# Performance work log

Measured on AMD Instinct MI355X. Metric: run time of the kernel, lower is better.

## Reference

```python
import jax, jax.numpy as jnp
import numpy as np

D_MODEL = 1024
N_HEADS = 16
HEAD_DIM = D_MODEL // N_HEADS
EPS = 1e-6


def setup_inputs() -> dict:
    key = jax.random.key(0)
    ks = jax.random.split(key, 5)
    b, s = 2, 2048
    x = jax.random.normal(ks[0], (b, s, D_MODEL), dtype=jnp.float32)
    scale = 1.0 / np.sqrt(D_MODEL)
    Wq = jax.random.normal(ks[1], (D_MODEL, D_MODEL), dtype=jnp.float32) * scale
    Wk = jax.random.normal(ks[2], (D_MODEL, D_MODEL), dtype=jnp.float32) * scale
    Wv = jax.random.normal(ks[3], (D_MODEL, D_MODEL), dtype=jnp.float32) * scale
    Wo = jax.random.normal(ks[4], (D_MODEL, D_MODEL), dtype=jnp.float32) * scale
    return {"x": x, "Wq": Wq, "Wk": Wk, "Wv": Wv, "Wo": Wo}


def _feature_map(t):
    return jax.nn.relu(t) + EPS


def reference(x, Wq, Wk, Wv, Wo):
    b, s, _ = x.shape
    # nn.Linear applies x @ W.T
    q = (x @ Wq.T).reshape(b, s, N_HEADS, HEAD_DIM)
    k = (x @ Wk.T).reshape(b, s, N_HEADS, HEAD_DIM)
    v = (x @ Wv.T).reshape(b, s, N_HEADS, HEAD_DIM)
    q = _feature_map(q).transpose(0, 2, 1, 3)  # bhsd
    k = _feature_map(k).transpose(0, 2, 1, 3)  # bhsd
    v = v.transpose(0, 2, 1, 3)                # bhsm
    # cumulative KV outer products: (b,h,s,d,m)
    kv = jnp.einsum('bhsd,bhsm->bhsdm', k, v)
    kv_cum = jnp.cumsum(kv, axis=2)
    out = jnp.einsum('bhsd,bhsdm->bhsm', q, kv_cum)
    k_cum = jnp.cumsum(k, axis=2)
    z = 1.0 / (jnp.einsum('bhsd,bhsd->bhs', q, k_cum) + EPS)
    out = out * z[..., None]
    out = out.transpose(0, 2, 1, 3).reshape(b, s, D_MODEL)
    return out @ Wo.T
```

## Files before the change

kernel.cpp:

```cpp
#include <hip/hip_runtime.h>

#define EPSF 1e-6f

typedef short bf16x8_t __attribute__((ext_vector_type(8)));
typedef float f32x4_t __attribute__((ext_vector_type(4)));

__device__ __forceinline__ ushort f2bf(float f) {
  union { float f; uint32_t u; } c; c.f = f;
  return (ushort)((c.u + 0x7FFFu + ((c.u >> 16) & 1u)) >> 16);
}
__device__ __forceinline__ float bf2f(ushort u) {
  union { uint32_t u; float f; } c; c.u = ((uint32_t)u) << 16;
  return c.f;
}

#define SWB(row, kbyte) (((row) << 7) + ((kbyte) ^ (((row) & 7) << 4)))

__global__ __launch_bounds__(256) void cvt5_kernel(
    const float4* __restrict__ x, const float4* __restrict__ wq,
    const float4* __restrict__ wk, const float4* __restrict__ wv,
    const float4* __restrict__ wo,
    ushort4* __restrict__ xb, ushort4* __restrict__ wqb,
    ushort4* __restrict__ wkb, ushort4* __restrict__ wvb,
    ushort4* __restrict__ wob)
{
  const int i = blockIdx.x * 256 + threadIdx.x;
  const float4* src; ushort4* dst; int off;
  if (i < (1 << 20)) { src = x; dst = xb; off = i; }
  else {
    const int j = i - (1 << 20);
    const int r = j >> 18;
    off = j & ((1 << 18) - 1);
    src = (r == 0) ? wq : (r == 1) ? wk : (r == 2) ? wv : wo;
    dst = (r == 0) ? wqb : (r == 1) ? wkb : (r == 2) ? wvb : wob;
  }
  const float4 v = src[off];
  ushort4 o;
  o.x = f2bf(v.x); o.y = f2bf(v.y); o.z = f2bf(v.z); o.w = f2bf(v.w);
  dst[off] = o;
}

template<int RELU, int OUT_BF16>
__device__ __forceinline__ void gemm_bt_mfma(
    const ushort* __restrict__ A, const ushort* __restrict__ B,
    void* __restrict__ C, const int K, const int N,
    const int row0, const int col0)
{
  __shared__ __align__(16) ushort As[2][128 * 32];
  __shared__ __align__(16) ushort Bs[2][128 * 32];
  const int tid = threadIdx.x;
  const int lane = tid & 63;
  const int wv = tid >> 6;
  const int wr = (wv >> 1) * 64;
  const int wc = (wv & 1) * 64;

  f32x4_t acc[4][4];
#pragma unroll
  for (int m = 0; m < 4; ++m)
#pragma unroll
    for (int n = 0; n < 4; ++n) acc[m][n] = (f32x4_t){0.f, 0.f, 0.f, 0.f};

  const int fr = lane & 15;
  const int kh = (lane >> 4) * 8;

  const int chunk0 = wv * 64 + lane;
  const int chunk1 = chunk0 + 256;
  const int rowA0 = chunk0 >> 2, kpA0 = (chunk0 & 3) << 3;
  const int rowA1 = chunk1 >> 2, kpA1 = (chunk1 & 3) << 3;
  const int ldoff0 = (wv * 64) * 8;
  const int ldoff1 = (wv * 64 + 256) * 8;

#define STAGE(buf, k0)                                                        \
  do {                                                                        \
    __builtin_amdgcn_global_load_lds(                                         \
        (const __attribute__((address_space(1))) void*)(A +                   \
            (size_t)(row0 + rowA0) * K + (k0) + kpA0),                        \
        (__attribute__((address_space(3))) void*)(&As[buf][ldoff0]), 16, 0, 0);\
    __builtin_amdgcn_global_load_lds(                                         \
        (const __attribute__((address_space(1))) void*)(B +                   \
            (size_t)(col0 + rowA0) * K + (k0) + kpA0),                        \
        (__attribute__((address_space(3))) void*)(&Bs[buf][ldoff0]), 16, 0, 0);\
    __builtin_amdgcn_global_load_lds(                                         \
        (const __attribute__((address_space(1))) void*)(A +                   \
            (size_t)(row0 + rowA1) * K + (k0) + kpA1),                        \
        (__attribute__((address_space(3))) void*)(&As[buf][ldoff1]), 16, 0, 0);\
    __builtin_amdgcn_global_load_lds(                                         \
        (const __attribute__((address_space(1))) void*)(B +                   \
            (size_t)(col0 + rowA1) * K + (k0) + kpA1),                        \
        (__attribute__((address_space(3))) void*)(&Bs[buf][ldoff1]), 16, 0, 0);\
  } while (0)

#define COMPUTE(buf)                                                          \
  do {                                                                        \
    bf16x8_t af[4], bfr[4];                                                   \
    _Pragma("unroll")                                                         \
    for (int m = 0; m < 4; ++m)                                               \
      af[m] = *(const bf16x8_t*)&As[buf][(wr + m * 16 + fr) * 32 + kh];       \
    _Pragma("unroll")                                                         \
    for (int n = 0; n < 4; ++n)                                               \
      bfr[n] = *(const bf16x8_t*)&Bs[buf][(wc + n * 16 + fr) * 32 + kh];      \
    __builtin_amdgcn_s_setprio(1);                                            \
    _Pragma("unroll")                                                         \
    for (int m = 0; m < 4; ++m)                                               \
      _Pragma("unroll")                                                       \
      for (int n = 0; n < 4; ++n)                                             \
        acc[m][n] = __builtin_amdgcn_mfma_f32_16x16x32_bf16(                  \
            af[m], bfr[n], acc[m][n], 0, 0, 0);                               \
    __builtin_amdgcn_s_setprio(0);                                            \
  } while (0)

  const int NT = K >> 5;
  STAGE(0, 0);
  __syncthreads();
  for (int t = 0; t < NT - 2; t += 2) {
    STAGE(1, (t + 1) << 5);
    COMPUTE(0);
    __syncthreads();
    STAGE(0, (t + 2) << 5);
    COMPUTE(1);
    __syncthreads();
  }
  STAGE(1, (NT - 1) << 5);
  COMPUTE(0);
  __syncthreads();
  COMPUTE(1);

#undef STAGE
#undef COMPUTE

  const int rq = (lane >> 4) * 4;
#pragma unroll
  for (int m = 0; m < 4; ++m) {
#pragma unroll
    for (int r = 0; r < 4; ++r) {
      const size_t grow = (size_t)(row0 + wr + m * 16 + rq + r);
#pragma unroll
      for (int n = 0; n < 4; ++n) {
        float val = acc[m][n][r];
        if (RELU) val = fmaxf(val, 0.f) + EPSF;
        const size_t gcol = (size_t)(col0 + wc + n * 16 + fr);
        if (OUT_BF16) ((ushort*)C)[grow * N + gcol] = f2bf(val);
        else          ((float*)C)[grow * N + gcol] = val;
      }
    }
  }
}

__global__ __launch_bounds__(256) void qkv_gemm_kernel(
    const ushort* __restrict__ xb,
    const ushort* __restrict__ wqb, const ushort* __restrict__ wkb,
    const ushort* __restrict__ wvb,
    ushort* __restrict__ q, ushort* __restrict__ k, ushort* __restrict__ v)
{
  const int which = blockIdx.y >> 3;
  const int bcol = blockIdx.y & 7;
  const ushort* B = (which == 0) ? wqb : (which == 1) ? wkb : wvb;
  ushort* C = (which == 0) ? q : (which == 1) ? k : v;
  if (which < 2)
    gemm_bt_mfma<1, 1>(xb, B, C, 1024, 1024, blockIdx.x * 128, bcol * 128);
  else
    gemm_bt_mfma<0, 1>(xb, B, C, 1024, 1024, blockIdx.x * 128, bcol * 128);
}

__global__ __launch_bounds__(256) void out_gemm_kernel(
    const ushort* __restrict__ at, const ushort* __restrict__ wob,
    float* __restrict__ out)
{
  gemm_bt_mfma<0, 0>(at, wob, out, 1024, 1024, blockIdx.x * 128, blockIdx.y * 128);
}


__global__ __launch_bounds__(256) void chunk_sums_kernel(
    const ushort* __restrict__ kbuf, const ushort* __restrict__ vbuf,
    float* __restrict__ kvsum, float* __restrict__ ksum)
{
  __shared__ __align__(16) ushort Kt[64 * 64];
  __shared__ __align__(16) ushort Vt[64 * 64];
  const int chunk = blockIdx.x;
  const int seq = blockIdx.y;
  const int b = seq >> 4, h = seq & 15;
  const int tid = threadIdx.x;
  const size_t base = ((size_t)b * 2048 + chunk * 64) * 1024 + h * 64;

#pragma unroll
  for (int r = 0; r < 2; ++r) {
    const int idx = tid + (r << 8);
    const int j = idx >> 3;
    const int e0 = (idx & 7) << 3;
    const bf16x8_t kv8 = *(const bf16x8_t*)(kbuf + base + (size_t)j * 1024 + e0);
    const bf16x8_t vv8 = *(const bf16x8_t*)(vbuf + base + (size_t)j * 1024 + e0);
#pragma unroll
    for (int t = 0; t < 8; ++t) {
      *(ushort*)((char*)Kt + SWB(e0 + t, j * 2)) = (ushort)kv8[t];
      *(ushort*)((char*)Vt + SWB(e0 + t, j * 2)) = (ushort)vv8[t];
    }
  }
  __syncthreads();

  if (tid < 64) {
    float s = 0.f;
#pragma unroll
    for (int g = 0; g < 8; ++g) {
      const bf16x8_t kr = *(const bf16x8_t*)((char*)Kt + SWB(tid, g * 16));
#pragma unroll
      for (int t = 0; t < 8; ++t) s += bf2f((ushort)kr[t]);
    }
    ksum[((size_t)seq * 32 + chunk) * 64 + tid] = s;
  }

  const int lane = tid & 63;
  const int wv = tid >> 6;
  const int wm = (wv >> 1) * 32;
  const int wd = (wv & 1) * 32;
  const int fr = lane & 15;
  const int khb = (lane >> 4) * 16;

  f32x4_t acc[2][2];
#pragma unroll
  for (int m = 0; m < 2; ++m)
#pragma unroll
    for (int n = 0; n < 2; ++n) acc[m][n] = (f32x4_t){0.f, 0.f, 0.f, 0.f};

#pragma unroll
  for (int kk = 0; kk < 2; ++kk) {
    bf16x8_t av[2], bk[2];
#pragma unroll
    for (int m = 0; m < 2; ++m)
      av[m] = *(const bf16x8_t*)((char*)Vt + SWB(wm + m * 16 + fr, kk * 64 + khb));
#pragma unroll
    for (int n = 0; n < 2; ++n)
      bk[n] = *(const bf16x8_t*)((char*)Kt + SWB(wd + n * 16 + fr, kk * 64 + khb));
#pragma unroll
    for (int m = 0; m < 2; ++m)
#pragma unroll
      for (int n = 0; n < 2; ++n)
        acc[m][n] = __builtin_amdgcn_mfma_f32_16x16x32_bf16(
            av[m], bk[n], acc[m][n], 0, 0, 0);
  }

  const size_t kvbase = ((size_t)seq * 32 + chunk) << 12;
  const int rq = (lane >> 4) * 4;
#pragma unroll
  for (int m = 0; m < 2; ++m)
#pragma unroll
    for (int r = 0; r < 4; ++r) {
      const int mrow = wm + m * 16 + rq + r;
#pragma unroll
      for (int n = 0; n < 2; ++n) {
        const int dcol = wd + n * 16 + fr;
        kvsum[kvbase + (size_t)mrow * 64 + dcol] = acc[m][n][r];
      }
    }
}

__global__ __launch_bounds__(256) void scan_kernel(
    float* __restrict__ kvsum, float* __restrict__ ksum)
{
  const int slice = blockIdx.x & 15;
  const int seq = blockIdx.x >> 4;
  const int e = slice * 256 + threadIdx.x;
  const size_t base = ((size_t)seq << 17) + e;
  float vals[32];
#pragma unroll
  for (int c = 0; c < 32; ++c) vals[c] = kvsum[base + ((size_t)c << 12)];
  float run = 0.f;
#pragma unroll
  for (int c = 0; c < 32; ++c) {
    const float t = vals[c];
    kvsum[base + ((size_t)c << 12)] = run;
    run += t;
  }
  if (slice == 0 && threadIdx.x < 64) {
    const size_t kb = (size_t)seq * 2048 + threadIdx.x;
    float kv2[32];
#pragma unroll
    for (int c = 0; c < 32; ++c) kv2[c] = ksum[kb + (size_t)c * 64];
    float run2 = 0.f;
#pragma unroll
    for (int c = 0; c < 32; ++c) {
      const float t = kv2[c];
      ksum[kb + (size_t)c * 64] = run2;
      run2 += t;
    }
  }
}

__global__ __launch_bounds__(256) void attn_chunk_kernel(
    const ushort* __restrict__ qbuf, const ushort* __restrict__ kbuf,
    const ushort* __restrict__ vbuf, const float* __restrict__ kvsum,
    const float* __restrict__ ksum, ushort* __restrict__ attn)
{
  __shared__ __align__(16) ushort Qs[64 * 64];
  __shared__ __align__(16) ushort Ks[64 * 64];
  __shared__ __align__(16) ushort Vt[64 * 64];
  __shared__ __align__(16) ushort Pl[64 * 64];
  __shared__ float ksp[64];
  __shared__ float zinv[64];
  const int chunk = blockIdx.x;
  const int seq = blockIdx.y;
  const int b = seq >> 4, h = seq & 15;
  const int tid = threadIdx.x;
  const size_t base = ((size_t)b * 2048 + chunk * 64) * 1024 + h * 64;

#pragma unroll
  for (int r = 0; r < 2; ++r) {
    const int idx = tid + (r << 8);
    const int row = idx >> 3;
    const int e0 = (idx & 7) << 3;
    const int kb = e0 << 1;
    *(bf16x8_t*)((char*)Qs + SWB(row, kb)) =
        *(const bf16x8_t*)(qbuf + base + (size_t)row * 1024 + e0);
    *(bf16x8_t*)((char*)Ks + SWB(row, kb)) =
        *(const bf16x8_t*)(kbuf + base + (size_t)row * 1024 + e0);
    const bf16x8_t vv8 = *(const bf16x8_t*)(vbuf + base + (size_t)row * 1024 + e0);
#pragma unroll
    for (int t = 0; t < 8; ++t)
      *(ushort*)((char*)Vt + SWB(e0 + t, row * 2)) = (ushort)vv8[t];
  }
  if (tid < 64) ksp[tid] = ksum[((size_t)seq * 32 + chunk) * 64 + tid];
  __syncthreads();

  const int lane = tid & 63;
  const int wv = tid >> 6;
  const int wr = (wv >> 1) * 32;
  const int wc = (wv & 1) * 32;
  const int fr = lane & 15;
  const int khb = (lane >> 4) * 16;
  const int rq = (lane >> 4) * 4;

  f32x4_t sf[2][2];
#pragma unroll
  for (int m = 0; m < 2; ++m)
#pragma unroll
    for (int n = 0; n < 2; ++n) sf[m][n] = (f32x4_t){0.f, 0.f, 0.f, 0.f};
#pragma unroll
  for (int kk = 0; kk < 2; ++kk) {
    bf16x8_t aq[2], bk[2];
#pragma unroll
    for (int m = 0; m < 2; ++m)
      aq[m] = *(const bf16x8_t*)((char*)Qs + SWB(wr + m * 16 + fr, kk * 64 + khb));
#pragma unroll
    for (int n = 0; n < 2; ++n)
      bk[n] = *(const bf16x8_t*)((char*)Ks + SWB(wc + n * 16 + fr, kk * 64 + khb));
#pragma unroll
    for (int m = 0; m < 2; ++m)
#pragma unroll
      for (int n = 0; n < 2; ++n)
        sf[m][n] = __builtin_amdgcn_mfma_f32_16x16x32_bf16(
            aq[m], bk[n], sf[m][n], 0, 0, 0);
  }
  __syncthreads();

#pragma unroll
  for (int m = 0; m < 2; ++m)
#pragma unroll
    for (int r = 0; r < 4; ++r) {
      const int i = wr + m * 16 + rq + r;
#pragma unroll
      for (int n = 0; n < 2; ++n) {
        const int j = wc + n * 16 + fr;
        const float pv = (j <= i) ? sf[m][n][r] : 0.f;
        *(ushort*)((char*)Pl + SWB(i, j * 2)) = f2bf(pv);
      }
    }
  const size_t kvbase = ((size_t)seq * 32 + chunk) << 12;
#pragma unroll
  for (int r = 0; r < 2; ++r) {
    const int idx = tid + (r << 8);
    const int mrow = idx >> 3;
    const int d0 = (idx & 7) << 3;
    const float4 lo = *(const float4*)(kvsum + kvbase + (size_t)mrow * 64 + d0);
    const float4 hi = *(const float4*)(kvsum + kvbase + (size_t)mrow * 64 + d0 + 4);
    bf16x8_t kv8;
    kv8[0] = (short)f2bf(lo.x); kv8[1] = (short)f2bf(lo.y);
    kv8[2] = (short)f2bf(lo.z); kv8[3] = (short)f2bf(lo.w);
    kv8[4] = (short)f2bf(hi.x); kv8[5] = (short)f2bf(hi.y);
    kv8[6] = (short)f2bf(hi.z); kv8[7] = (short)f2bf(hi.w);
    *(bf16x8_t*)((char*)Ks + SWB(mrow, d0 << 1)) = kv8;
  }
  __syncthreads();

  if (tid < 64) {
    const int i = tid;
    float dsum = 0.f, ssum = 0.f;
#pragma unroll
    for (int g = 0; g < 8; ++g) {
      const bf16x8_t qr = *(const bf16x8_t*)((char*)Qs + SWB(i, g * 16));
      const bf16x8_t pr = *(const bf16x8_t*)((char*)Pl + SWB(i, g * 16));
#pragma unroll
      for (int t = 0; t < 8; ++t) {
        dsum = fmaf(bf2f((ushort)qr[t]), ksp[g * 8 + t], dsum);
        ssum += bf2f((ushort)pr[t]);
      }
    }
    zinv[i] = 1.f / (dsum + ssum + EPSF);
  }

  f32x4_t of[2][2];
#pragma unroll
  for (int m = 0; m < 2; ++m)
#pragma unroll
    for (int n = 0; n < 2; ++n) of[m][n] = (f32x4_t){0.f, 0.f, 0.f, 0.f};
#pragma unroll
  for (int kk = 0; kk < 2; ++kk) {
    bf16x8_t ap[2], bv[2];
#pragma unroll
    for (int m = 0; m < 2; ++m)
      ap[m] = *(const bf16x8_t*)((char*)Pl + SWB(wr + m * 16 + fr, kk * 64 + khb));
#pragma unroll
    for (int n = 0; n < 2; ++n)
      bv[n] = *(const bf16x8_t*)((char*)Vt + SWB(wc + n * 16 + fr, kk * 64 + khb));
#pragma unroll
    for (int m = 0; m < 2; ++m)
#pragma unroll
      for (int n = 0; n < 2; ++n)
        of[m][n] = __builtin_amdgcn_mfma_f32_16x16x32_bf16(
            ap[m], bv[n], of[m][n], 0, 0, 0);
  }
#pragma unroll
  for (int kk = 0; kk < 2; ++kk) {
    bf16x8_t aq[2], bkv[2];
#pragma unroll
    for (int m = 0; m < 2; ++m)
      aq[m] = *(const bf16x8_t*)((char*)Qs + SWB(wr + m * 16 + fr, kk * 64 + khb));
#pragma unroll
    for (int n = 0; n < 2; ++n)
      bkv[n] = *(const bf16x8_t*)((char*)Ks + SWB(wc + n * 16 + fr, kk * 64 + khb));
#pragma unroll
    for (int m = 0; m < 2; ++m)
#pragma unroll
      for (int n = 0; n < 2; ++n)
        of[m][n] = __builtin_amdgcn_mfma_f32_16x16x32_bf16(
            aq[m], bkv[n], of[m][n], 0, 0, 0);
  }
  __syncthreads();

#pragma unroll
  for (int m = 0; m < 2; ++m)
#pragma unroll
    for (int r = 0; r < 4; ++r) {
      const int i = wr + m * 16 + rq + r;
      const float z = zinv[i];
#pragma unroll
      for (int n = 0; n < 2; ++n) {
        const int mcol = wc + n * 16 + fr;
        attn[base + (size_t)i * 1024 + mcol] = f2bf(of[m][n][r] * z);
      }
    }
}

extern "C" void kernel_launch(void* const* d_in, const int* in_sizes, int n_in,
                              void* d_out, int out_size, void* d_ws, size_t ws_size,
                              hipStream_t stream)
{
  (void)in_sizes; (void)n_in; (void)out_size; (void)ws_size;
  const float* x  = (const float*)d_in[0];
  const float* Wq = (const float*)d_in[1];
  const float* Wk = (const float*)d_in[2];
  const float* Wv = (const float*)d_in[3];
  const float* Wo = (const float*)d_in[4];
  float* out = (float*)d_out;

  const size_t NM = (size_t)4096 * 1024;
  ushort* xb  = (ushort*)d_ws;
  ushort* wqb = xb + NM;
  ushort* wkb = wqb + (1 << 20);
  ushort* wvb = wkb + (1 << 20);
  ushort* wob = wvb + (1 << 20);
  ushort* qb  = wob + (1 << 20);
  ushort* kb  = qb + NM;
  ushort* vb  = kb + NM;
  ushort* at  = vb + NM;
  float*  ksm = (float*)(at + NM);
  float*  kvs = (float*)d_out;

  cvt5_kernel<<<8192, 256, 0, stream>>>(
      (const float4*)x, (const float4*)Wq, (const float4*)Wk,
      (const float4*)Wv, (const float4*)Wo,
      (ushort4*)xb, (ushort4*)wqb, (ushort4*)wkb, (ushort4*)wvb, (ushort4*)wob);
  qkv_gemm_kernel<<<dim3(32, 24), 256, 0, stream>>>(xb, wqb, wkb, wvb, qb, kb, vb);
  chunk_sums_kernel<<<dim3(32, 32), 256, 0, stream>>>(kb, vb, kvs, ksm);
  scan_kernel<<<512, 256, 0, stream>>>(kvs, ksm);
  attn_chunk_kernel<<<dim3(32, 32), 256, 0, stream>>>(qb, kb, vb, kvs, ksm, at);
  out_gemm_kernel<<<dim3(32, 8), 256, 0, stream>>>(at, wob, out);
}
```

Before: 180.7 us.

## Use 64-wide swizzled K tiles in GEMMs and split-K the output projection

The shared GEMM helper now stages K tiles of 64 instead of 32, using an XOR-swizzled LDS layout to avoid bank conflicts, which halves the number of barriers per K loop. The output projection is split along K into two halves across a new grid dimension, and partial results are combined with float atomicAdd into an output that is zeroed beforehand with a memset. This doubles the block count for the under-occupied 256-block output GEMM. The cost is atomic traffic, an extra memset, a different workspace location for the KV sums (moved off d_out), and doubled LDS per block, which may reduce occupancy.

```diff
diff --git a/kernel.cpp b/kernel.cpp
--- a/kernel.cpp
+++ b/kernel.cpp
@@ -40,14 +40,15 @@
   dst[off] = o;
 }
 
-template<int RELU, int OUT_BF16>
+template<int RELU, int OUT_BF16, int ATOMIC>
 __device__ __forceinline__ void gemm_bt_mfma(
     const ushort* __restrict__ A, const ushort* __restrict__ B,
-    void* __restrict__ C, const int K, const int N,
-    const int row0, const int col0)
-{
-  __shared__ __align__(16) ushort As[2][128 * 32];
-  __shared__ __align__(16) ushort Bs[2][128 * 32];
+    void* __restrict__ C, const int K,
+    const int kbeg, const int kend,
+    const int N, const int row0, const int col0)
+{
+  __shared__ __align__(16) ushort As[2][128 * 64];
+  __shared__ __align__(16) ushort Bs[2][128 * 64];
   const int tid = threadIdx.x;
   const int lane = tid & 63;
   const int wv = tid >> 6;
@@ -61,66 +62,72 @@
     for (int n = 0; n < 4; ++n) acc[m][n] = (f32x4_t){0.f, 0.f, 0.f, 0.f};
 
   const int fr = lane & 15;
-  const int kh = (lane >> 4) * 8;
-
-  const int chunk0 = wv * 64 + lane;
-  const int chunk1 = chunk0 + 256;
-  const int rowA0 = chunk0 >> 2, kpA0 = (chunk0 & 3) << 3;
-  const int rowA1 = chunk1 >> 2, kpA1 = (chunk1 & 3) << 3;
-  const int ldoff0 = (wv * 64) * 8;
-  const int ldoff1 = (wv * 64 + 256) * 8;
-
-#define STAGE(buf, k0)                                                        \
+
+  int rowc[4], scol[4], dsto[4];
+#pragma unroll
+  for (int is = 0; is < 4; ++is) {
+    const int c0 = is * 256 + tid;
+    rowc[is] = c0 >> 3;
+    scol[is] = (((c0 & 7) ^ ((c0 >> 3) & 7)) << 3);
+    dsto[is] = ((c0 >> 6) << 6) * 8;
+  }
+
+#define STAGE(buf, k0v)                                                       \
   do {                                                                        \
-    __builtin_amdgcn_global_load_lds(                                         \
-        (const __attribute__((address_space(1))) void*)(A +                   \
-            (size_t)(row0 + rowA0) * K + (k0) + kpA0),                        \
-        (__attribute__((address_space(3))) void*)(&As[buf][ldoff0]), 16, 0, 0);\
-    __builtin_amdgcn_global_load_lds(                                         \
-        (const __attribute__((address_space(1))) void*)(B +                   \
-            (size_t)(col0 + rowA0) * K + (k0) + kpA0),                        \
-        (__attribute__((address_space(3))) void*)(&Bs[buf][ldoff0]), 16, 0, 0);\
-    __builtin_amdgcn_global_load_lds(                                         \
-        (const __attribute__((address_space(1))) void*)(A +                   \
-            (size_t)(row0 + rowA1) * K + (k0) + kpA1),                        \
-        (__attribute__((address_space(3))) void*)(&As[buf][ldoff1]), 16, 0, 0);\
-    __builtin_amdgcn_global_load_lds(                                         \
-        (const __attribute__((address_space(1))) void*)(B +                   \
-            (size_t)(col0 + rowA1) * K + (k0) + kpA1),                        \
-        (__attribute__((address_space(3))) void*)(&Bs[buf][ldoff1]), 16, 0, 0);\
+    _Pragma("unroll")                                                         \
+    for (int is = 0; is < 4; ++is) {                                          \
+      __builtin_amdgcn_global_load_lds(                                       \
+          (const __attribute__((address_space(1))) void*)(A +                 \
+              (size_t)(row0 + rowc[is]) * K + (k0v) + scol[is]),              \
+          (__attribute__((address_space(3))) void*)(&As[buf][dsto[is]]),      \
+          16, 0, 0);                                                          \
+      __builtin_amdgcn_global_load_lds(                                       \
+          (const __attribute__((address_space(1))) void*)(B +                 \
+              (size_t)(col0 + rowc[is]) * K + (k0v) + scol[is]),              \
+          (__attribute__((address_space(3))) void*)(&Bs[buf][dsto[is]]),      \
+          16, 0, 0);                                                          \
+    }                                                                         \
   } while (0)
 
 #define COMPUTE(buf)                                                          \
   do {                                                                        \
-    bf16x8_t af[4], bfr[4];                                                   \
     _Pragma("unroll")                                                         \
-    for (int m = 0; m < 4; ++m)                                               \
-      af[m] = *(const bf16x8_t*)&As[buf][(wr + m * 16 + fr) * 32 + kh];       \
-    _Pragma("unroll")                                                         \
-    for (int n = 0; n < 4; ++n)                                               \
-      bfr[n] = *(const bf16x8_t*)&Bs[buf][(wc + n * 16 + fr) * 32 + kh];      \
-    __builtin_amdgcn_s_setprio(1);                                            \
-    _Pragma("unroll")                                                         \
-    for (int m = 0; m < 4; ++m)                                               \
+    for (int kk = 0; kk < 2; ++kk) {                                          \
+      bf16x8_t af[4], bfr[4];                                                 \
+      const int kb = kk * 64 + (lane & 48);                                   \
       _Pragma("unroll")                                                       \
-      for (int n = 0; n < 4; ++n)                                             \
-        acc[m][n] = __builtin_amdgcn_mfma_f32_16x16x32_bf16(                  \
-            af[m], bfr[n], acc[m][n], 0, 0, 0);                               \
-    __builtin_amdgcn_s_setprio(0);                                            \
+      for (int m = 0; m < 4; ++m) {                                           \
+        const int r_ = wr + m * 16 + fr;                                      \
+        af[m] = *(const bf16x8_t*)((const char*)As[buf] + SWB(r_, kb));       \
+      }                                                                       \
+      _Pragma("unroll")                                                       \
+      for (int n = 0; n < 4; ++n) {                                           \
+        const int r_ = wc + n * 16 + fr;                                      \
+        bfr[n] = *(const bf16x8_t*)((const char*)Bs[buf] + SWB(r_, kb));      \
+      }                                                                       \
+      __builtin_amdgcn_s_setprio(1);                                          \
+      _Pragma("unroll")                                                       \
+      for (int m = 0; m < 4; ++m)                                             \
+        _Pragma("unroll")                                                     \
+        for (int n = 0; n < 4; ++n)                                           \
+          acc[m][n] = __builtin_amdgcn_mfma_f32_16x16x32_bf16(                \
+              af[m], bfr[n], acc[m][n], 0, 0, 0);                             \
+      __builtin_amdgcn_s_setprio(0);                                          \
+    }                                                                         \
   } while (0)
 
-  const int NT = K >> 5;
-  STAGE(0, 0);
+  const int NT = (kend - kbeg) >> 6;
+  STAGE(0, kbeg);
   __syncthreads();
   for (int t = 0; t < NT - 2; t += 2) {
-    STAGE(1, (t + 1) << 5);
+    STAGE(1, kbeg + ((t + 1) << 6));
     COMPUTE(0);
     __syncthreads();
-    STAGE(0, (t + 2) << 5);
+    STAGE(0, kbeg + ((t + 2) << 6));
     COMPUTE(1);
     __syncthreads();
   }
-  STAGE(1, (NT - 1) << 5);
+  STAGE(1, kbeg + ((NT - 1) << 6));
   COMPUTE(0);
   __syncthreads();
   COMPUTE(1);
@@ -139,8 +146,9 @@
         float val = acc[m][n][r];
         if (RELU) val = fmaxf(val, 0.f) + EPSF;
         const size_t gcol = (size_t)(col0 + wc + n * 16 + fr);
-        if (OUT_BF16) ((ushort*)C)[grow * N + gcol] = f2bf(val);
-        else          ((float*)C)[grow * N + gcol] = val;
+        if (ATOMIC)        atomicAdd(&((float*)C)[grow * N + gcol], val);
+        else if (OUT_BF16) ((ushort*)C)[grow * N + gcol] = f2bf(val);
+        else               ((float*)C)[grow * N + gcol] = val;
       }
     }
   }
@@ -157,16 +165,20 @@
   const ushort* B = (which == 0) ? wqb : (which == 1) ? wkb : wvb;
   ushort* C = (which == 0) ? q : (which == 1) ? k : v;
   if (which < 2)
-    gemm_bt_mfma<1, 1>(xb, B, C, 1024, 1024, blockIdx.x * 128, bcol * 128);
+    gemm_bt_mfma<1, 1, 0>(xb, B, C, 1024, 0, 1024, 1024,
+                          blockIdx.x * 128, bcol * 128);
   else
-    gemm_bt_mfma<0, 1>(xb, B, C, 1024, 1024, blockIdx.x * 128, bcol * 128);
+    gemm_bt_mfma<0, 1, 0>(xb, B, C, 1024, 0, 1024, 1024,
+                          blockIdx.x * 128, bcol * 128);
 }
 
 __global__ __launch_bounds__(256) void out_gemm_kernel(
     const ushort* __restrict__ at, const ushort* __restrict__ wob,
     float* __restrict__ out)
 {
-  gemm_bt_mfma<0, 0>(at, wob, out, 1024, 1024, blockIdx.x * 128, blockIdx.y * 128);
+  const int kb0 = blockIdx.z * 512;
+  gemm_bt_mfma<0, 0, 1>(at, wob, out, 1024, kb0, kb0 + 512, 1024,
+                        blockIdx.x * 128, blockIdx.y * 128);
 }
 
 
@@ -453,7 +465,7 @@
                               void* d_out, int out_size, void* d_ws, size_t ws_size,
                               hipStream_t stream)
 {
-  (void)in_sizes; (void)n_in; (void)out_size; (void)ws_size;
+  (void)in_sizes; (void)n_in; (void)ws_size;
   const float* x  = (const float*)d_in[0];
   const float* Wq = (const float*)d_in[1];
   const float* Wk = (const float*)d_in[2];
@@ -472,7 +484,9 @@
   ushort* vb  = kb + NM;
   ushort* at  = vb + NM;
   float*  ksm = (float*)(at + NM);
-  float*  kvs = (float*)d_out;
+  float*  kvs = ksm + 65536;
+
+  hipMemsetAsync(d_out, 0, (size_t)out_size * sizeof(float), stream);
 
   cvt5_kernel<<<8192, 256, 0, stream>>>(
       (const float4*)x, (const float4*)Wq, (const float4*)Wk,
@@ -482,5 +496,5 @@
   chunk_sums_kernel<<<dim3(32, 32), 256, 0, stream>>>(kb, vb, kvs, ksm);
   scan_kernel<<<512, 256, 0, stream>>>(kvs, ksm);
   attn_chunk_kernel<<<dim3(32, 32), 256, 0, stream>>>(qb, kb, vb, kvs, ksm, at);
-  out_gemm_kernel<<<dim3(32, 8), 256, 0, stream>>>(at, wob, out);
-}
+  out_gemm_kernel<<<dim3(32, 8, 2), 256, 0, stream>>>(at, wob, out);
+}
```

After: 199.5 us. 1.1x slower.

## Store scanned KV prefix as bf16 and narrow out-GEMM tile to 128x64

Applied to the files above, without the earlier changes.

The scan kernel now writes the exclusive KV prefix sums directly as bf16 into a separate workspace buffer. The attention kernel therefore loads half the bytes and skips its per-element conversion. The output projection uses a 128x64 tile with twice as many blocks, giving more parallelism on a GPU with many CUs. The change also removes the setprio hints around the MFMA loop and turns the ReLU flag into a runtime bool, which merges the two QKV template instantiations but adds a branch in the epilogue.

```diff
diff --git a/kernel.cpp b/kernel.cpp
--- a/kernel.cpp
+++ b/kernel.cpp
@@ -40,73 +40,71 @@
   dst[off] = o;
 }
 
-template<int RELU, int OUT_BF16>
+template<int BN, int OUT_BF16>
 __device__ __forceinline__ void gemm_bt_mfma(
     const ushort* __restrict__ A, const ushort* __restrict__ B,
-    void* __restrict__ C, const int K, const int N,
-    const int row0, const int col0)
-{
-  __shared__ __align__(16) ushort As[2][128 * 32];
-  __shared__ __align__(16) ushort Bs[2][128 * 32];
+    void* __restrict__ C, const int K,
+    const int N, const int row0, const int col0, const bool relu)
+{
+  constexpr int NFR = BN / 32;
+  __shared__ __align__(16) uint As[2][2048];
+  __shared__ __align__(16) uint Bs[2][BN * 16];
   const int tid = threadIdx.x;
   const int lane = tid & 63;
   const int wv = tid >> 6;
   const int wr = (wv >> 1) * 64;
-  const int wc = (wv & 1) * 64;
-
-  f32x4_t acc[4][4];
+  const int wc = (wv & 1) * (BN / 2);
+
+  f32x4_t acc[4][NFR];
 #pragma unroll
   for (int m = 0; m < 4; ++m)
 #pragma unroll
-    for (int n = 0; n < 4; ++n) acc[m][n] = (f32x4_t){0.f, 0.f, 0.f, 0.f};
+    for (int n = 0; n < NFR; ++n) acc[m][n] = (f32x4_t){0.f, 0.f, 0.f, 0.f};
 
   const int fr = lane & 15;
   const int kh = (lane >> 4) * 8;
 
-  const int chunk0 = wv * 64 + lane;
-  const int chunk1 = chunk0 + 256;
-  const int rowA0 = chunk0 >> 2, kpA0 = (chunk0 & 3) << 3;
-  const int rowA1 = chunk1 >> 2, kpA1 = (chunk1 & 3) << 3;
-  const int ldoff0 = (wv * 64) * 8;
-  const int ldoff1 = (wv * 64 + 256) * 8;
-
-#define STAGE(buf, k0)                                                        \
+#define STAGE(buf, k0v)                                                       \
   do {                                                                        \
-    __builtin_amdgcn_global_load_lds(                                         \
-        (const __attribute__((address_space(1))) void*)(A +                   \
-            (size_t)(row0 + rowA0) * K + (k0) + kpA0),                        \
-        (__attribute__((address_space(3))) void*)(&As[buf][ldoff0]), 16, 0, 0);\
-    __builtin_amdgcn_global_load_lds(                                         \
-        (const __attribute__((address_space(1))) void*)(B +                   \
-            (size_t)(col0 + rowA0) * K + (k0) + kpA0),                        \
-        (__attribute__((address_space(3))) void*)(&Bs[buf][ldoff0]), 16, 0, 0);\
-    __builtin_amdgcn_global_load_lds(                                         \
-        (const __attribute__((address_space(1))) void*)(A +                   \
-            (size_t)(row0 + rowA1) * K + (k0) + kpA1),                        \
-        (__attribute__((address_space(3))) void*)(&As[buf][ldoff1]), 16, 0, 0);\
-    __builtin_amdgcn_global_load_lds(                                         \
-        (const __attribute__((address_space(1))) void*)(B +                   \
-            (size_t)(col0 + rowA1) * K + (k0) + kpA1),                        \
-        (__attribute__((address_space(3))) void*)(&Bs[buf][ldoff1]), 16, 0, 0);\
+    _Pragma("unroll")                                                         \
+    for (int is = 0; is < 2; ++is) {                                          \
+      const int c = tid + (is << 8);                                          \
+      const int row = c >> 2, kq = (c & 3) << 3;                              \
+      __builtin_amdgcn_global_load_lds(                                       \
+          (const __attribute__((address_space(1))) void*)(A +                 \
+              (size_t)(row0 + row) * K + (k0v) + kq),                         \
+          (__attribute__((address_space(3))) void*)(&As[buf][(c & ~63) * 4]), \
+          16, 0, 0);                                                          \
+    }                                                                         \
+    _Pragma("unroll")                                                         \
+    for (int is = 0; is < BN / 64; ++is) {                                    \
+      const int c = tid + (is << 8);                                          \
+      const int row = c >> 2, kq = (c & 3) << 3;                              \
+      __builtin_amdgcn_global_load_lds(                                       \
+          (const __attribute__((address_space(1))) void*)(B +                 \
+              (size_t)(col0 + row) * K + (k0v) + kq),                         \
+          (__attribute__((address_space(3))) void*)(&Bs[buf][(c & ~63) * 4]), \
+          16, 0, 0);                                                          \
+    }                                                                         \
   } while (0)
 
 #define COMPUTE(buf)                                                          \
   do {                                                                        \
-    bf16x8_t af[4], bfr[4];                                                   \
+    bf16x8_t af[4], bfr[NFR];                                                 \
     _Pragma("unroll")                                                         \
     for (int m = 0; m < 4; ++m)                                               \
-      af[m] = *(const bf16x8_t*)&As[buf][(wr + m * 16 + fr) * 32 + kh];       \
+      af[m] = *(const bf16x8_t*)((const ushort*)As[buf] +                     \
+                                 (size_t)(wr + m * 16 + fr) * 32 + kh);       \
     _Pragma("unroll")                                                         \
-    for (int n = 0; n < 4; ++n)                                               \
-      bfr[n] = *(const bf16x8_t*)&Bs[buf][(wc + n * 16 + fr) * 32 + kh];      \
-    __builtin_amdgcn_s_setprio(1);                                            \
+    for (int n = 0; n < NFR; ++n)                                             \
+      bfr[n] = *(const bf16x8_t*)((const ushort*)Bs[buf] +                    \
+                                  (size_t)(wc + n * 16 + fr) * 32 + kh);      \
     _Pragma("unroll")                                                         \
     for (int m = 0; m < 4; ++m)                                               \
       _Pragma("unroll")                                                       \
-      for (int n = 0; n < 4; ++n)                                             \
+      for (int n = 0; n < NFR; ++n)                                           \
         acc[m][n] = __builtin_amdgcn_mfma_f32_16x16x32_bf16(                  \
             af[m], bfr[n], acc[m][n], 0, 0, 0);                               \
-    __builtin_amdgcn_s_setprio(0);                                            \
   } while (0)
 
   const int NT = K >> 5;
@@ -135,9 +133,9 @@
     for (int r = 0; r < 4; ++r) {
       const size_t grow = (size_t)(row0 + wr + m * 16 + rq + r);
 #pragma unroll
-      for (int n = 0; n < 4; ++n) {
+      for (int n = 0; n < NFR; ++n) {
         float val = acc[m][n][r];
-        if (RELU) val = fmaxf(val, 0.f) + EPSF;
+        if (relu) val = fmaxf(val, 0.f) + EPSF;
         const size_t gcol = (size_t)(col0 + wc + n * 16 + fr);
         if (OUT_BF16) ((ushort*)C)[grow * N + gcol] = f2bf(val);
         else          ((float*)C)[grow * N + gcol] = val;
@@ -156,17 +154,16 @@
   const int bcol = blockIdx.y & 7;
   const ushort* B = (which == 0) ? wqb : (which == 1) ? wkb : wvb;
   ushort* C = (which == 0) ? q : (which == 1) ? k : v;
-  if (which < 2)
-    gemm_bt_mfma<1, 1>(xb, B, C, 1024, 1024, blockIdx.x * 128, bcol * 128);
-  else
-    gemm_bt_mfma<0, 1>(xb, B, C, 1024, 1024, blockIdx.x * 128, bcol * 128);
+  gemm_bt_mfma<128, 1>(xb, B, C, 1024, 1024,
+                       blockIdx.x * 128, bcol * 128, which < 2);
 }
 
 __global__ __launch_bounds__(256) void out_gemm_kernel(
     const ushort* __restrict__ at, const ushort* __restrict__ wob,
     float* __restrict__ out)
 {
-  gemm_bt_mfma<0, 0>(at, wob, out, 1024, 1024, blockIdx.x * 128, blockIdx.y * 128);
+  gemm_bt_mfma<64, 0>(at, wob, out, 1024, 1024,
+                      blockIdx.x * 128, blockIdx.y * 64, false);
 }
 
 
@@ -174,8 +171,8 @@
     const ushort* __restrict__ kbuf, const ushort* __restrict__ vbuf,
     float* __restrict__ kvsum, float* __restrict__ ksum)
 {
-  __shared__ __align__(16) ushort Kt[64 * 64];
-  __shared__ __align__(16) ushort Vt[64 * 64];
+  __shared__ __align__(16) uint Kt[2048];
+  __shared__ __align__(16) uint Vt[2048];
   const int chunk = blockIdx.x;
   const int seq = blockIdx.y;
   const int b = seq >> 4, h = seq & 15;
@@ -254,7 +251,8 @@
 }
 
 __global__ __launch_bounds__(256) void scan_kernel(
-    float* __restrict__ kvsum, float* __restrict__ ksum)
+    const float* __restrict__ kvsum, ushort* __restrict__ kvsb,
+    float* __restrict__ ksum)
 {
   const int slice = blockIdx.x & 15;
   const int seq = blockIdx.x >> 4;
@@ -266,9 +264,8 @@
   float run = 0.f;
 #pragma unroll
   for (int c = 0; c < 32; ++c) {
-    const float t = vals[c];
-    kvsum[base + ((size_t)c << 12)] = run;
-    run += t;
+    kvsb[base + ((size_t)c << 12)] = f2bf(run);
+    run += vals[c];
   }
   if (slice == 0 && threadIdx.x < 64) {
     const size_t kb = (size_t)seq * 2048 + threadIdx.x;
@@ -287,13 +284,13 @@
 
 __global__ __launch_bounds__(256) void attn_chunk_kernel(
     const ushort* __restrict__ qbuf, const ushort* __restrict__ kbuf,
-    const ushort* __restrict__ vbuf, const float* __restrict__ kvsum,
+    const ushort* __restrict__ vbuf, const ushort* __restrict__ kvsb,
     const float* __restrict__ ksum, ushort* __restrict__ attn)
 {
-  __shared__ __align__(16) ushort Qs[64 * 64];
-  __shared__ __align__(16) ushort Ks[64 * 64];
-  __shared__ __align__(16) ushort Vt[64 * 64];
-  __shared__ __align__(16) ushort Pl[64 * 64];
+  __shared__ __align__(16) uint Qs[2048];
+  __shared__ __align__(16) uint Ks[2048];
+  __shared__ __align__(16) uint Vt[2048];
+  __shared__ __align__(16) uint Pl[2048];
   __shared__ float ksp[64];
   __shared__ float zinv[64];
   const int chunk = blockIdx.x;
@@ -369,13 +366,7 @@
     const int idx = tid + (r << 8);
     const int mrow = idx >> 3;
     const int d0 = (idx & 7) << 3;
-    const float4 lo = *(const float4*)(kvsum + kvbase + (size_t)mrow * 64 + d0);
-    const float4 hi = *(const float4*)(kvsum + kvbase + (size_t)mrow * 64 + d0 + 4);
-    bf16x8_t kv8;
-    kv8[0] = (short)f2bf(lo.x); kv8[1] = (short)f2bf(lo.y);
-    kv8[2] = (short)f2bf(lo.z); kv8[3] = (short)f2bf(lo.w);
-    kv8[4] = (short)f2bf(hi.x); kv8[5] = (short)f2bf(hi.y);
-    kv8[6] = (short)f2bf(hi.z); kv8[7] = (short)f2bf(hi.w);
+    const bf16x8_t kv8 = *(const bf16x8_t*)(kvsb + kvbase + (size_t)mrow * 64 + d0);
     *(bf16x8_t*)((char*)Ks + SWB(mrow, d0 << 1)) = kv8;
   }
   __syncthreads();
@@ -472,7 +463,8 @@
   ushort* vb  = kb + NM;
   ushort* at  = vb + NM;
   float*  ksm = (float*)(at + NM);
-  float*  kvs = (float*)d_out;
+  float*  kvs = ksm + 65536;
+  ushort* kvsb = (ushort*)(kvs + NM);
 
   cvt5_kernel<<<8192, 256, 0, stream>>>(
       (const float4*)x, (const float4*)Wq, (const float4*)Wk,
@@ -480,7 +472,7 @@
       (ushort4*)xb, (ushort4*)wqb, (ushort4*)wkb, (ushort4*)wvb, (ushort4*)wob);
   qkv_gemm_kernel<<<dim3(32, 24), 256, 0, stream>>>(xb, wqb, wkb, wvb, qb, kb, vb);
   chunk_sums_kernel<<<dim3(32, 32), 256, 0, stream>>>(kb, vb, kvs, ksm);
-  scan_kernel<<<512, 256, 0, stream>>>(kvs, ksm);
-  attn_chunk_kernel<<<dim3(32, 32), 256, 0, stream>>>(qb, kb, vb, kvs, ksm, at);
-  out_gemm_kernel<<<dim3(32, 8), 256, 0, stream>>>(at, wob, out);
-}
+  scan_kernel<<<512, 256, 0, stream>>>(kvs, kvsb, ksm);
+  attn_chunk_kernel<<<dim3(32, 32), 256, 0, stream>>>(qb, kb, vb, kvsb, ksm, at);
+  out_gemm_kernel<<<dim3(32, 16), 256, 0, stream>>>(at, wob, out);
+}
```

Result: faster. 175.3 us (-3.0%).
